# Kernel tuning notes

Measured on AMD Instinct MI355X. Metric: run time of the kernel, lower is better.

## Reference

```python
import jax, jax.numpy as jnp
import numpy as np

THRESHOLD = 0.2  # relation_threshold default
LN_EPS = 1e-5


def setup_inputs() -> dict:
    key = jax.random.key(0)
    ks = jax.random.split(key, 4)
    N1, N2, F, H, R = 256, 256, 512, 512, 4
    feats_img = jax.random.normal(ks[0], (N1, F), dtype=jnp.float32)
    feats_txt = jax.random.normal(ks[1], (N2, F), dtype=jnp.float32)
    # relation_projector params (R stacked copies of the 2-layer MLP)
    W1 = jax.random.normal(ks[2], (R, H, 2 * F), dtype=jnp.float32) / np.sqrt(2 * F)
    b1 = jnp.zeros((R, H), dtype=jnp.float32)
    gamma = jnp.ones((R, H), dtype=jnp.float32)
    beta = jnp.zeros((R, H), dtype=jnp.float32)
    w2 = jax.random.normal(ks[3], (R, H), dtype=jnp.float32) / np.sqrt(H)
    b2 = jnp.zeros((R,), dtype=jnp.float32)
    return {"feats_img": feats_img, "feats_txt": feats_txt, "W1": W1, "b1": b1,
            "gamma": gamma, "beta": beta, "w2": w2, "b2": b2}


def _relation_scores(x, W1, b1, gamma, beta, w2, b2):
    """Vectorized pairwise MLP: for each relation r, score[i,j] = MLP_r(cat(x_i, x_j)).
    Returns [N, N, R]."""
    N, F = x.shape
    R = W1.shape[0]
    Wl, Wr = W1[:, :, :F], W1[:, :, F:]  # Linear on concat = left half @ x_i + right half @ x_j
    scores = []
    for r in range(R):  # small fixed loop over relations keeps peak memory at one [N,N,H] block
        a = x @ Wl[r].T                                  # [N, H]
        b = x @ Wr[r].T                                  # [N, H]
        h = a[:, None, :] + b[None, :, :] + b1[r]        # [N, N, H]
        mu = h.mean(-1, keepdims=True)
        var = h.var(-1, keepdims=True)                   # biased var, matches torch LayerNorm
        hn = (h - mu) * jax.lax.rsqrt(var + LN_EPS) * gamma[r] + beta[r]
        s = jnp.maximum(hn, 0.0) @ w2[r] + b2[r]         # [N, N]
        scores.append(s)
    return jnp.stack(scores, axis=-1)                    # [N, N, R]


def reference(feats_img, feats_txt, W1, b1, gamma, beta, w2, b2):
    # node_features = cat over modalities (node_types is a static host-side list: omitted)
    x = jnp.concatenate([feats_img, feats_txt], axis=0)  # [N, F]
    S = _relation_scores(x, W1, b1, gamma, beta, w2, b2) # [N, N, R]
    best_rel = jnp.argmax(S, axis=-1).astype(jnp.int32)  # edge_types, dense form
    best_score = S.max(axis=-1)                          # edge_weights, dense form
    N = x.shape[0]
    diag = jnp.eye(N, dtype=bool)
    edge_mask = (~diag) & (best_score > THRESHOLD)       # dense encoding of edge_index
    return x, best_score, best_rel, edge_mask
```

## Files before the change

### kernel.cpp

```cpp
#include <hip/hip_runtime.h>
#include <math.h>


typedef __attribute__((ext_vector_type(8))) short s8b;
typedef __attribute__((ext_vector_type(4))) float f32x4;
typedef __attribute__((ext_vector_type(4))) unsigned short us4;

namespace {
constexpr size_t PLANE  = 512 * 512;
constexpr size_t OFF_A   = 0;
constexpr size_t OFF_B   = OFF_A + 4 * PLANE;
constexpr size_t OFF_DOT = OFF_B + 4 * PLANE;
constexpr size_t OFF_S   = OFF_DOT + 8 * PLANE;
constexpr size_t OFF_MA  = OFF_S + 8 * PLANE;
constexpr size_t OFF_QA  = OFF_MA + 2048;
constexpr size_t OFF_MB  = OFF_QA + 2048;
constexpr size_t OFF_QB  = OFF_MB + 2048;
constexpr size_t OFF_G   = OFF_QB + 2048;
constexpr size_t OFF_BW  = OFF_G + 2048;
constexpr size_t OFF_SA  = OFF_BW + 4096;
constexpr size_t OFF_SB  = OFF_SA + 2048;
constexpr size_t OFF_CB  = OFF_SB + 2048;
}

__device__ __forceinline__ unsigned short bf16rne(float v) {
  const unsigned u = __float_as_uint(v);
  return (unsigned short)((u + 0x7fffu + ((u >> 16) & 1u)) >> 16);
}

__device__ __forceinline__ f32x4 mfma16(s8b a, s8b b, f32x4 c) {
  return __builtin_amdgcn_mfma_f32_16x16x32_bf16(a, b, c, 0, 0, 0);
}

__global__ __launch_bounds__(256) void k0_gemm(const float* __restrict__ img,
                                               const float* __restrict__ txt,
                                               const float* __restrict__ W1,
                                               const float* __restrict__ b1,
                                               float* __restrict__ ws) {
  const int b = blockIdx.x;
  const int it = b >> 6;
  const int ct = b & 63;
  const int which = ct >> 5;
  const int r = (ct >> 3) & 3;
  const int ht = ct & 7;
  const int i0 = it << 6, h0 = ht << 6;
  const int t = threadIdx.x;
  const int tx = t & 15, ty = t >> 4;

  __shared__ float Xs[16 * 68];
  __shared__ float Wsm[16 * 68];

  float acc[16], pacc[16];
#pragma unroll
  for (int p = 0; p < 16; ++p) { acc[p] = 0.f; pacc[p] = 0.f; }

  const int srow = t >> 2;
  const int sf4 = (t & 3) << 2;
  const int xi = i0 + srow;
  const float* xrow = (xi < 256) ? (img + (size_t)xi * 512)
                                 : (txt + (size_t)(xi - 256) * 512);
  const float* wrow = W1 + (size_t)(r * 512 + h0 + srow) * 1024 + which * 512;

  for (int k0 = 0; k0 < 512; k0 += 16) {
    const float4 xv = *(const float4*)(xrow + k0 + sf4);
    const float4 wv = *(const float4*)(wrow + k0 + sf4);
    __syncthreads();
    Xs[(sf4 + 0) * 68 + srow] = xv.x;
    Xs[(sf4 + 1) * 68 + srow] = xv.y;
    Xs[(sf4 + 2) * 68 + srow] = xv.z;
    Xs[(sf4 + 3) * 68 + srow] = xv.w;
    Wsm[(sf4 + 0) * 68 + srow] = wv.x;
    Wsm[(sf4 + 1) * 68 + srow] = wv.y;
    Wsm[(sf4 + 2) * 68 + srow] = wv.z;
    Wsm[(sf4 + 3) * 68 + srow] = wv.w;
    __syncthreads();
#pragma unroll
    for (int k = 0; k < 16; ++k) {
      const float4 a4 = *(const float4*)&Xs[k * 68 + 4 * ty];
      const float4 b4 = *(const float4*)&Wsm[k * 68 + 4 * tx];
      const float av[4] = {a4.x, a4.y, a4.z, a4.w};
      const float bv[4] = {b4.x, b4.y, b4.z, b4.w};
#pragma unroll
      for (int c = 0; c < 4; ++c)
#pragma unroll
        for (int d = 0; d < 4; ++d)
          pacc[c * 4 + d] = fmaf(av[c], bv[d], pacc[c * 4 + d]);
    }
#pragma unroll
    for (int p = 0; p < 16; ++p) { acc[p] += pacc[p]; pacc[p] = 0.f; }
  }

  float4 bb = make_float4(0.f, 0.f, 0.f, 0.f);
  if (which) bb = *(const float4*)(b1 + r * 512 + h0 + 4 * tx);
  float* dst = ws + (which ? OFF_B : OFF_A) + (size_t)r * PLANE;
#pragma unroll
  for (int c = 0; c < 4; ++c) {
    float4 v;
    v.x = acc[c * 4 + 0] + bb.x;
    v.y = acc[c * 4 + 1] + bb.y;
    v.z = acc[c * 4 + 2] + bb.z;
    v.w = acc[c * 4 + 3] + bb.w;
    *(float4*)(dst + (size_t)(i0 + 4 * ty + c) * 512 + h0 + 4 * tx) = v;
  }
}

__global__ __launch_bounds__(256) void k_conv2(float* __restrict__ ws) {
  const int idx = blockIdx.x * 256 + threadIdx.x;
  const float4 v = *(const float4*)(ws + (size_t)idx * 4);
  unsigned short* SH = (unsigned short*)(ws + OFF_S);
  unsigned short *dh, *dl;
  if (idx < 262144) {
    const size_t e = (size_t)idx * 4;
    dh = SH + e;                 dl = SH + 4 * PLANE + e;
  } else {
    const size_t e = (size_t)idx * 4 - 4 * PLANE;
    dh = SH + 8 * PLANE + e;     dl = SH + 12 * PLANE + e;
  }
  const float vv[4] = {v.x, v.y, v.z, v.w};
  us4 h4, l4;
#pragma unroll
  for (int c = 0; c < 4; ++c) {
    const unsigned short hh = bf16rne(vv[c]);
    h4[c] = hh;
    l4[c] = bf16rne(vv[c] - __uint_as_float(((unsigned)hh) << 16));
  }
  *(us4*)dh = h4;
  *(us4*)dl = l4;
}

__global__ __launch_bounds__(256) void k1_stats(float* __restrict__ ws,
                                                const float* __restrict__ gamma,
                                                const float* __restrict__ beta,
                                                const float* __restrict__ w2) {
  const int t = threadIdx.x;
  const int gw = (blockIdx.x * 256 + t) >> 6;
  const int lane = t & 63;
  const int which = gw >> 11;
  const int rr = (gw >> 9) & 3;
  const int row = gw & 511;
  const float* src =
      ws + (which ? OFF_B : OFF_A) + (size_t)(rr * 512 + row) * 512 + lane * 8;
  const float* gsrc = gamma + rr * 512 + lane * 8;
  const float* wsrc = w2 + rr * 512 + lane * 8;
  float s = 0.f, q = 0.f, sa = 0.f, cgs = 0.f;
#pragma unroll
  for (int c = 0; c < 2; ++c) {
    const float4 v = *(const float4*)(src + c * 4);
    const float4 g = *(const float4*)(gsrc + c * 4);
    const float4 w = *(const float4*)(wsrc + c * 4);
    s += v.x + v.y + v.z + v.w;
    q += v.x * v.x + v.y * v.y + v.z * v.z + v.w * v.w;
    const float cgx = 0.5f * w.x * g.x;
    const float cgy = 0.5f * w.y * g.y;
    const float cgz = 0.5f * w.z * g.z;
    const float cgw = 0.5f * w.w * g.w;
    sa += cgx * v.x + cgy * v.y + cgz * v.z + cgw * v.w;
    cgs += cgx + cgy + cgz + cgw;
  }
#pragma unroll
  for (int off = 32; off >= 1; off >>= 1) {
    s += __shfl_down(s, off, 64);
    q += __shfl_down(q, off, 64);
    sa += __shfl_down(sa, off, 64);
    cgs += __shfl_down(cgs, off, 64);
  }
  if (lane == 0) {
    const float ma = s * (1.f / 512.f);
    ws[(which ? OFF_MB : OFF_MA) + rr * 512 + row] = ma;
    ws[(which ? OFF_QB : OFF_QA) + rr * 512 + row] = q;
    ws[(which ? OFF_SB : OFF_SA) + rr * 512 + row] = sa - ma * cgs;
  }
  if (blockIdx.x < 8) {
    const int idx = blockIdx.x * 256 + t;
    ws[OFF_G + idx] = gamma[idx];
    float2 bw;
    bw.x = beta[idx];
    bw.y = 0.5f * w2[idx];
    *(float2*)(ws + OFF_BW + (size_t)idx * 2) = bw;
  }
  if (blockIdx.x == 8) {
    const int rb = t >> 6;
    float cb = 0.f;
#pragma unroll
    for (int c = 0; c < 8; ++c)
      cb += 0.5f * w2[rb * 512 + lane * 8 + c] * beta[rb * 512 + lane * 8 + c];
#pragma unroll
    for (int off = 32; off >= 1; off >>= 1) cb += __shfl_down(cb, off, 64);
    if (lane == 0) ws[OFF_CB + rb] = cb;
  }
}

__global__ __launch_bounds__(256) void k2_mfma(float* __restrict__ ws) {
  const int b = blockIdx.x;
  const int jt = b & 7, it = (b >> 3) & 7, r = (b >> 6) & 3, ks = b >> 8;
  const int i0 = it << 6, j0 = jt << 6;
  const int kb = ks << 8;
  const int t = threadIdx.x, w = t >> 6, l = t & 63;
  const int wr = w >> 1, wc = w & 1;
  const int lrow = l & 15, lk = (l >> 4) << 3;

  const unsigned short* SH = (const unsigned short*)(ws + OFF_S);
  const unsigned short* AH = SH;
  const unsigned short* AL = SH + 4 * PLANE;
  const unsigned short* BH = SH + 8 * PLANE;
  const unsigned short* BL = SH + 12 * PLANE;

  const int ia = i0 + wr * 32 + lrow;
  const int jb = j0 + wc * 32 + lrow;
  const size_t ar0 = (size_t)(r * 512 + ia) * 512 + kb + lk;
  const size_t ar1 = ar0 + 16 * 512;
  const size_t br0 = (size_t)(r * 512 + jb) * 512 + kb + lk;
  const size_t br1 = br0 + 16 * 512;

  f32x4 acc00 = {0.f, 0.f, 0.f, 0.f}, acc01 = acc00, acc10 = acc00, acc11 = acc00;

#pragma unroll
  for (int k0 = 0; k0 < 256; k0 += 32) {
    const s8b ah0 = *(const s8b*)(AH + ar0 + k0);
    const s8b ah1 = *(const s8b*)(AH + ar1 + k0);
    const s8b al0 = *(const s8b*)(AL + ar0 + k0);
    const s8b al1 = *(const s8b*)(AL + ar1 + k0);
    const s8b bh0 = *(const s8b*)(BH + br0 + k0);
    const s8b bh1 = *(const s8b*)(BH + br1 + k0);
    const s8b bl0 = *(const s8b*)(BL + br0 + k0);
    const s8b bl1 = *(const s8b*)(BL + br1 + k0);
    acc00 = mfma16(ah0, bh0, acc00);
    acc00 = mfma16(ah0, bl0, acc00);
    acc00 = mfma16(al0, bh0, acc00);
    acc01 = mfma16(ah0, bh1, acc01);
    acc01 = mfma16(ah0, bl1, acc01);
    acc01 = mfma16(al0, bh1, acc01);
    acc10 = mfma16(ah1, bh0, acc10);
    acc10 = mfma16(ah1, bl0, acc10);
    acc10 = mfma16(al1, bh0, acc10);
    acc11 = mfma16(ah1, bh1, acc11);
    acc11 = mfma16(ah1, bl1, acc11);
    acc11 = mfma16(al1, bh1, acc11);
  }

  float* dst = ws + OFF_DOT + (size_t)ks * (4 * PLANE) + (size_t)r * PLANE;
  const int rb = i0 + wr * 32 + ((l >> 4) << 2);
  const int cb = j0 + wc * 32 + lrow;
#pragma unroll
  for (int v = 0; v < 4; ++v) {
    dst[(size_t)(rb + v) * 512 + cb]           = acc00[v];
    dst[(size_t)(rb + v) * 512 + cb + 16]      = acc01[v];
    dst[(size_t)(rb + 16 + v) * 512 + cb]      = acc10[v];
    dst[(size_t)(rb + 16 + v) * 512 + cb + 16] = acc11[v];
  }
}

__global__ __launch_bounds__(256) void k3_score(float* __restrict__ ws) {
  const int b = blockIdx.x;
  const int jt = b & 15, it = (b >> 4) & 7, r = (b >> 7) & 3, ks = b >> 9;
  const int i0 = it << 6, j0 = jt << 5;
  const int t = threadIdx.x;
  const int tx = t & 15, ty = t >> 4;

  __shared__ float As2[64 * 68];
  __shared__ float Bs2[64 * 36];
  __shared__ float bwS[64 * 2];

  const float4 mav = *(const float4*)(ws + OFF_MA + r * 512 + i0 + 4 * ty);
  const float4 qav = *(const float4*)(ws + OFF_QA + r * 512 + i0 + 4 * ty);
  const float2 mbv = *(const float2*)(ws + OFF_MB + r * 512 + j0 + 2 * tx);
  const float2 qbv = *(const float2*)(ws + OFF_QB + r * 512 + j0 + 2 * tx);
  const float4 sav = *(const float4*)(ws + OFF_SA + r * 512 + i0 + 4 * ty);
  const float2 sbv = *(const float2*)(ws + OFF_SB + r * 512 + j0 + 2 * tx);
  const float cbr = ws[OFF_CB + r];
  const float mavA[4] = {mav.x, mav.y, mav.z, mav.w};
  const float qavA[4] = {qav.x, qav.y, qav.z, qav.w};
  const float savA[4] = {sav.x, sav.y, sav.z, sav.w};
  const float mbA[2] = {mbv.x, mbv.y};
  const float qbA[2] = {qbv.x, qbv.y};
  const float sbA[2] = {sbv.x, sbv.y};
  float Sv[8], acc[8];
#pragma unroll
  for (int c = 0; c < 4; ++c) {
    const size_t doff = (size_t)r * PLANE + (size_t)(i0 + 4 * ty + c) * 512 + j0 + 2 * tx;
    const float2 d0 = *(const float2*)(ws + OFF_DOT + doff);
    const float2 d1 = *(const float2*)(ws + OFF_DOT + 4 * PLANE + doff);
    const float dA[2] = {d0.x + d1.x, d0.y + d1.y};
#pragma unroll
    for (int d = 0; d < 2; ++d) {
      const int p = c * 2 + d;
      const float mu = mavA[c] + mbA[d];
      const float msq = (qavA[c] + qbA[d] + 2.f * dA[d]) * (1.f / 512.f);
      const float var = msq - mu * mu;
      Sv[p] = 1.0f / sqrtf(var + 1e-5f);
      acc[p] = (ks == 0) ? fmaf(Sv[p], savA[c] + sbA[d], cbr) : 0.f;
    }
  }

  const int kbase = ks << 8;
  const int srow = ty;
  const int sf4 = tx << 2;
  const int sblk = tx & 7;
  float maR[4], mbR[2];
#pragma unroll
  for (int c2 = 0; c2 < 4; ++c2)
    maR[c2] = ws[OFF_MA + r * 512 + i0 + srow + 16 * c2];
#pragma unroll
  for (int c2 = 0; c2 < 2; ++c2)
    mbR[c2] = ws[OFF_MB + r * 512 + j0 + srow + 16 * c2];

  float4 aC[4], bC[2], gC;
  float2 bwC = make_float2(0.f, 0.f);
  {
    const int kb = kbase;
    gC = *(const float4*)(ws + OFF_G + r * 512 + kb + sf4);
#pragma unroll
    for (int c2 = 0; c2 < 4; ++c2)
      aC[c2] = *(const float4*)(ws + OFF_A + (size_t)(r * 512 + i0 + srow + 16 * c2) * 512 + kb + sf4);
#pragma unroll
    for (int c2 = 0; c2 < 2; ++c2)
      bC[c2] = *(const float4*)(ws + OFF_B + (size_t)(r * 512 + j0 + srow + 16 * c2) * 512 + kb + sf4);
    if (t < 64) bwC = *(const float2*)(ws + OFF_BW + (size_t)(r * 512 + kb + t) * 2);
  }

#pragma unroll
  for (int kc = 0; kc < 4; ++kc) {
    __syncthreads();
    {
      const float ga[4] = {gC.x, gC.y, gC.z, gC.w};
#pragma unroll
      for (int c2 = 0; c2 < 4; ++c2) {
        const int row = srow + 16 * c2;
        const int off = (((row >> 2) ^ sblk) << 2) + (row & 3);
        const float aq[4] = {aC[c2].x, aC[c2].y, aC[c2].z, aC[c2].w};
#pragma unroll
        for (int q = 0; q < 4; ++q)
          As2[(sf4 + q) * 68 + off] = (aq[q] - maR[c2]) * ga[q];
      }
#pragma unroll
      for (int c2 = 0; c2 < 2; ++c2) {
        const int row = srow + 16 * c2;
        const int off = (((row >> 2) ^ sblk) << 2) + (row & 3);
        const float bq[4] = {bC[c2].x, bC[c2].y, bC[c2].z, bC[c2].w};
#pragma unroll
        for (int q = 0; q < 4; ++q)
          Bs2[(sf4 + q) * 36 + off] = (bq[q] - mbR[c2]) * ga[q];
      }
      if (t < 64) *(float2*)(bwS + 2 * t) = bwC;
    }
    if (kc < 3) {
      const int kb = kbase + ((kc + 1) << 6);
      gC = *(const float4*)(ws + OFF_G + r * 512 + kb + sf4);
#pragma unroll
      for (int c2 = 0; c2 < 4; ++c2)
        aC[c2] = *(const float4*)(ws + OFF_A + (size_t)(r * 512 + i0 + srow + 16 * c2) * 512 + kb + sf4);
#pragma unroll
      for (int c2 = 0; c2 < 2; ++c2)
        bC[c2] = *(const float4*)(ws + OFF_B + (size_t)(r * 512 + j0 + srow + 16 * c2) * 512 + kb + sf4);
      if (t < 64) bwC = *(const float2*)(ws + OFF_BW + (size_t)(r * 512 + kb + t) * 2);
    }
    __syncthreads();

    float cacc[8];
#pragma unroll
    for (int p = 0; p < 8; ++p) cacc[p] = 0.f;

#pragma unroll 4
    for (int k = 0; k < 64; ++k) {
      const int K = (k >> 2) & 7;
      const float4 aA = *(const float4*)&As2[k * 68 + ((ty ^ K) << 2)];
      const float2 bB = *(const float2*)&Bs2[k * 36 + (((tx >> 1) ^ K) << 2) + ((tx & 1) << 1)];
      const float2 bw = *(const float2*)&bwS[2 * k];
      const float aq[4] = {aA.x, aA.y, aA.z, aA.w};
      const float bq[2] = {bB.x, bB.y};
#pragma unroll
      for (int c = 0; c < 4; ++c)
#pragma unroll
        for (int d = 0; d < 2; ++d) {
          const int p = c * 2 + d;
          const float u = aq[c] + bq[d];
          const float hn = fmaf(u, Sv[p], bw.x);
          cacc[p] = fmaf(bw.y, fabsf(hn), cacc[p]);
        }
    }
#pragma unroll
    for (int p = 0; p < 8; ++p) acc[p] += cacc[p];
  }

  float* dst = ws + OFF_S + (size_t)ks * (4 * PLANE) + (size_t)r * PLANE;
#pragma unroll
  for (int c = 0; c < 4; ++c) {
    float2 v;
    v.x = acc[c * 2 + 0];
    v.y = acc[c * 2 + 1];
    *(float2*)(dst + (size_t)(i0 + 4 * ty + c) * 512 + j0 + 2 * tx) = v;
  }
}

__global__ __launch_bounds__(256) void k4_combine(const float* __restrict__ ws,
                                                  const float* __restrict__ img,
                                                  const float* __restrict__ txt,
                                                  const float* __restrict__ b2,
                                                  float* __restrict__ out) {
  const int idx = blockIdx.x * 256 + threadIdx.x;
  const int i = idx >> 9, j = idx & 511;
  const float* s0 = ws + OFF_S;
  const float* s1 = ws + OFF_S + 4 * PLANE;
  float best = -3.4e38f;
  int rel = 0;
#pragma unroll
  for (int r = 0; r < 4; ++r) {
    const float s = s0[r * PLANE + idx] + s1[r * PLANE + idx] + b2[r];
    if (s > best) { best = s; rel = r; }
  }
  out[idx] = (i < 256) ? img[idx] : txt[idx - 131072];
  out[PLANE + idx] = best;
  out[2 * PLANE + idx] = (float)rel;
  out[3 * PLANE + idx] = (i != j && (double)best > 0.2) ? 1.0f : 0.0f;
}

extern "C" void kernel_launch(void* const* d_in, const int* in_sizes, int n_in,
                              void* d_out, int out_size, void* d_ws, size_t ws_size,
                              hipStream_t stream) {
  const float* img   = (const float*)d_in[0];
  const float* txt   = (const float*)d_in[1];
  const float* W1    = (const float*)d_in[2];
  const float* b1    = (const float*)d_in[3];
  const float* gamma = (const float*)d_in[4];
  const float* beta  = (const float*)d_in[5];
  const float* w2    = (const float*)d_in[6];
  const float* b2    = (const float*)d_in[7];
  float* ws  = (float*)d_ws;
  float* out = (float*)d_out;
  (void)in_sizes; (void)n_in; (void)out_size; (void)ws_size;

  hipLaunchKernelGGL(k0_gemm,    dim3(512),  dim3(256), 0, stream, img, txt, W1, b1, ws);
  hipLaunchKernelGGL(k_conv2,    dim3(2048), dim3(256), 0, stream, ws);
  hipLaunchKernelGGL(k1_stats,   dim3(1024), dim3(256), 0, stream, ws, gamma, beta, w2);
  hipLaunchKernelGGL(k2_mfma,    dim3(512),  dim3(256), 0, stream, ws);
  hipLaunchKernelGGL(k3_score,   dim3(1024), dim3(256), 0, stream, ws);
  hipLaunchKernelGGL(k4_combine, dim3(1024), dim3(256), 0, stream, ws, img, txt, b2, out);
}
```

Baseline: 192.7 us.

## Replace FP32 projection GEMM with split-bf16 MFMA and fuse hi/lo conversion

The scalar FP32 shared-memory GEMM that computes the left and right projections is replaced by a bf16 MFMA kernel. The inputs are split three ways (hi/mid/lo) and six cross-product MFMAs are accumulated to approximate FP32 accuracy. The kernel writes the hi/lo bf16 split of its outputs directly, so the separate conversion pass over the projections is dropped. In exchange it adds pre-conversion kernels for W1 and x that write extra bf16 planes to the workspace, and runs the projection as two launches, one per half of W1.

```diff
diff --git a/kernel.cpp b/kernel.cpp
--- a/kernel.cpp
+++ b/kernel.cpp
@@ -32,100 +32,160 @@
   return __builtin_amdgcn_mfma_f32_16x16x32_bf16(a, b, c, 0, 0, 0);
 }
 
-__global__ __launch_bounds__(256) void k0_gemm(const float* __restrict__ img,
-                                               const float* __restrict__ txt,
-                                               const float* __restrict__ W1,
-                                               const float* __restrict__ b1,
-                                               float* __restrict__ ws) {
-  const int b = blockIdx.x;
-  const int it = b >> 6;
-  const int ct = b & 63;
-  const int which = ct >> 5;
-  const int r = (ct >> 3) & 3;
-  const int ht = ct & 7;
-  const int i0 = it << 6, h0 = ht << 6;
-  const int t = threadIdx.x;
-  const int tx = t & 15, ty = t >> 4;
-
-  __shared__ float Xs[16 * 68];
-  __shared__ float Wsm[16 * 68];
-
-  float acc[16], pacc[16];
-#pragma unroll
-  for (int p = 0; p < 16; ++p) { acc[p] = 0.f; pacc[p] = 0.f; }
-
-  const int srow = t >> 2;
-  const int sf4 = (t & 3) << 2;
-  const int xi = i0 + srow;
-  const float* xrow = (xi < 256) ? (img + (size_t)xi * 512)
-                                 : (txt + (size_t)(xi - 256) * 512);
-  const float* wrow = W1 + (size_t)(r * 512 + h0 + srow) * 1024 + which * 512;
-
-  for (int k0 = 0; k0 < 512; k0 += 16) {
-    const float4 xv = *(const float4*)(xrow + k0 + sf4);
-    const float4 wv = *(const float4*)(wrow + k0 + sf4);
-    __syncthreads();
-    Xs[(sf4 + 0) * 68 + srow] = xv.x;
-    Xs[(sf4 + 1) * 68 + srow] = xv.y;
-    Xs[(sf4 + 2) * 68 + srow] = xv.z;
-    Xs[(sf4 + 3) * 68 + srow] = xv.w;
-    Wsm[(sf4 + 0) * 68 + srow] = wv.x;
-    Wsm[(sf4 + 1) * 68 + srow] = wv.y;
-    Wsm[(sf4 + 2) * 68 + srow] = wv.z;
-    Wsm[(sf4 + 3) * 68 + srow] = wv.w;
-    __syncthreads();
-#pragma unroll
-    for (int k = 0; k < 16; ++k) {
-      const float4 a4 = *(const float4*)&Xs[k * 68 + 4 * ty];
-      const float4 b4 = *(const float4*)&Wsm[k * 68 + 4 * tx];
-      const float av[4] = {a4.x, a4.y, a4.z, a4.w};
-      const float bv[4] = {b4.x, b4.y, b4.z, b4.w};
-#pragma unroll
-      for (int c = 0; c < 4; ++c)
-#pragma unroll
-        for (int d = 0; d < 4; ++d)
-          pacc[c * 4 + d] = fmaf(av[c], bv[d], pacc[c * 4 + d]);
-    }
-#pragma unroll
-    for (int p = 0; p < 16; ++p) { acc[p] += pacc[p]; pacc[p] = 0.f; }
-  }
-
-  float4 bb = make_float4(0.f, 0.f, 0.f, 0.f);
-  if (which) bb = *(const float4*)(b1 + r * 512 + h0 + 4 * tx);
-  float* dst = ws + (which ? OFF_B : OFF_A) + (size_t)r * PLANE;
-#pragma unroll
-  for (int c = 0; c < 4; ++c) {
-    float4 v;
-    v.x = acc[c * 4 + 0] + bb.x;
-    v.y = acc[c * 4 + 1] + bb.y;
-    v.z = acc[c * 4 + 2] + bb.z;
-    v.w = acc[c * 4 + 3] + bb.w;
-    *(float4*)(dst + (size_t)(i0 + 4 * ty + c) * 512 + h0 + 4 * tx) = v;
-  }
-}
-
-__global__ __launch_bounds__(256) void k_conv2(float* __restrict__ ws) {
+__global__ __launch_bounds__(256) void k_conv1a(const float* __restrict__ img,
+                                                const float* __restrict__ txt,
+                                                const float* __restrict__ W1,
+                                                float* __restrict__ ws) {
   const int idx = blockIdx.x * 256 + threadIdx.x;
-  const float4 v = *(const float4*)(ws + (size_t)idx * 4);
-  unsigned short* SH = (unsigned short*)(ws + OFF_S);
-  unsigned short *dh, *dl;
+  unsigned short* WPH = (unsigned short*)(ws + OFF_DOT);
+  float4 v;
+  size_t off;
+  unsigned short *dh, *dm, *dl;
   if (idx < 262144) {
-    const size_t e = (size_t)idx * 4;
-    dh = SH + e;                 dl = SH + 4 * PLANE + e;
+    const int row = idx >> 7, c4 = (idx & 127) << 2;
+    v = *(const float4*)(W1 + (size_t)row * 1024 + c4);
+    off = (size_t)row * 512 + c4;
+    dh = WPH; dm = WPH + 4 * PLANE; dl = WPH + 8 * PLANE;
   } else {
-    const size_t e = (size_t)idx * 4 - 4 * PLANE;
-    dh = SH + 8 * PLANE + e;     dl = SH + 12 * PLANE + e;
+    const int xi = idx - 262144;
+    v = (xi < 32768) ? ((const float4*)img)[xi] : ((const float4*)txt)[xi - 32768];
+    off = (size_t)xi * 4;
+    dh = WPH + 12 * PLANE; dm = WPH + 13 * PLANE; dl = WPH + 14 * PLANE;
   }
   const float vv[4] = {v.x, v.y, v.z, v.w};
-  us4 h4, l4;
+  us4 h4, m4, l4;
 #pragma unroll
   for (int c = 0; c < 4; ++c) {
     const unsigned short hh = bf16rne(vv[c]);
+    const float r1 = vv[c] - __uint_as_float(((unsigned)hh) << 16);
+    const unsigned short mm = bf16rne(r1);
+    const float r2 = r1 - __uint_as_float(((unsigned)mm) << 16);
     h4[c] = hh;
-    l4[c] = bf16rne(vv[c] - __uint_as_float(((unsigned)hh) << 16));
-  }
-  *(us4*)dh = h4;
-  *(us4*)dl = l4;
+    m4[c] = mm;
+    l4[c] = bf16rne(r2);
+  }
+  *(us4*)(dh + off) = h4;
+  *(us4*)(dm + off) = m4;
+  *(us4*)(dl + off) = l4;
+}
+
+__global__ __launch_bounds__(256) void k_conv1b(const float* __restrict__ W1,
+                                                float* __restrict__ ws) {
+  const int idx = blockIdx.x * 256 + threadIdx.x;
+  unsigned short* WPH = (unsigned short*)(ws + OFF_DOT);
+  const int row = idx >> 7, c4 = (idx & 127) << 2;
+  const float4 v = *(const float4*)(W1 + (size_t)row * 1024 + 512 + c4);
+  const size_t off = (size_t)row * 512 + c4;
+  const float vv[4] = {v.x, v.y, v.z, v.w};
+  us4 h4, m4, l4;
+#pragma unroll
+  for (int c = 0; c < 4; ++c) {
+    const unsigned short hh = bf16rne(vv[c]);
+    const float r1 = vv[c] - __uint_as_float(((unsigned)hh) << 16);
+    const unsigned short mm = bf16rne(r1);
+    const float r2 = r1 - __uint_as_float(((unsigned)mm) << 16);
+    h4[c] = hh;
+    m4[c] = mm;
+    l4[c] = bf16rne(r2);
+  }
+  *(us4*)(WPH + off) = h4;
+  *(us4*)(WPH + 4 * PLANE + off) = m4;
+  *(us4*)(WPH + 8 * PLANE + off) = l4;
+}
+
+__global__ __launch_bounds__(256) void k0_mfma(const float* __restrict__ b1,
+                                               float* __restrict__ ws, int which) {
+  const int b = blockIdx.x;
+  const int it = b >> 5, ct = b & 31;
+  const int r = ct >> 3, ht = ct & 7;
+  const int i0 = it << 6, h0 = ht << 6;
+  const int t = threadIdx.x, w = t >> 6, l = t & 63;
+  const int wr = w >> 1, wc = w & 1;
+  const int lrow = l & 15, lk = (l >> 4) << 3;
+
+  const unsigned short* WPH = (const unsigned short*)(ws + OFF_DOT);
+  const unsigned short* WPM = WPH + 4 * PLANE;
+  const unsigned short* WPL = WPH + 8 * PLANE;
+  const unsigned short* XPH = WPH + 12 * PLANE;
+  const unsigned short* XPM = WPH + 13 * PLANE;
+  const unsigned short* XPL = WPH + 14 * PLANE;
+
+  const int ia = i0 + wr * 32 + lrow;
+  const int hb = h0 + wc * 32 + lrow;
+  const size_t xr0 = (size_t)ia * 512 + lk;
+  const size_t xr1 = xr0 + 16 * 512;
+  const size_t wr0 = (size_t)(r * 512 + hb) * 512 + lk;
+  const size_t wr1 = wr0 + 16 * 512;
+
+  f32x4 acc00 = {0.f, 0.f, 0.f, 0.f}, acc01 = acc00, acc10 = acc00, acc11 = acc00;
+
+#pragma unroll 4
+  for (int k0 = 0; k0 < 512; k0 += 32) {
+    const s8b xh0 = *(const s8b*)(XPH + xr0 + k0);
+    const s8b xh1 = *(const s8b*)(XPH + xr1 + k0);
+    const s8b xm0 = *(const s8b*)(XPM + xr0 + k0);
+    const s8b xm1 = *(const s8b*)(XPM + xr1 + k0);
+    const s8b xl0 = *(const s8b*)(XPL + xr0 + k0);
+    const s8b xl1 = *(const s8b*)(XPL + xr1 + k0);
+    const s8b wh0 = *(const s8b*)(WPH + wr0 + k0);
+    const s8b wh1 = *(const s8b*)(WPH + wr1 + k0);
+    const s8b wm0 = *(const s8b*)(WPM + wr0 + k0);
+    const s8b wm1 = *(const s8b*)(WPM + wr1 + k0);
+    const s8b wl0 = *(const s8b*)(WPL + wr0 + k0);
+    const s8b wl1 = *(const s8b*)(WPL + wr1 + k0);
+    acc00 = mfma16(xh0, wh0, acc00);
+    acc00 = mfma16(xh0, wm0, acc00);
+    acc00 = mfma16(xm0, wh0, acc00);
+    acc00 = mfma16(xh0, wl0, acc00);
+    acc00 = mfma16(xm0, wm0, acc00);
+    acc00 = mfma16(xl0, wh0, acc00);
+    acc01 = mfma16(xh0, wh1, acc01);
+    acc01 = mfma16(xh0, wm1, acc01);
+    acc01 = mfma16(xm0, wh1, acc01);
+    acc01 = mfma16(xh0, wl1, acc01);
+    acc01 = mfma16(xm0, wm1, acc01);
+    acc01 = mfma16(xl0, wh1, acc01);
+    acc10 = mfma16(xh1, wh0, acc10);
+    acc10 = mfma16(xh1, wm0, acc10);
+    acc10 = mfma16(xm1, wh0, acc10);
+    acc10 = mfma16(xh1, wl0, acc10);
+    acc10 = mfma16(xm1, wm0, acc10);
+    acc10 = mfma16(xl1, wh0, acc10);
+    acc11 = mfma16(xh1, wh1, acc11);
+    acc11 = mfma16(xh1, wm1, acc11);
+    acc11 = mfma16(xm1, wh1, acc11);
+    acc11 = mfma16(xh1, wl1, acc11);
+    acc11 = mfma16(xm1, wm1, acc11);
+    acc11 = mfma16(xl1, wh1, acc11);
+  }
+
+  float bb0 = 0.f, bb1 = 0.f;
+  if (which) { bb0 = b1[r * 512 + hb]; bb1 = b1[r * 512 + hb + 16]; }
+  float* dst = ws + (which ? OFF_B : OFF_A) + (size_t)r * PLANE;
+  unsigned short* SHb = (unsigned short*)(ws + OFF_S) + (which ? 8 * PLANE : 0);
+  const int rb = i0 + wr * 32 + ((l >> 4) << 2);
+  const int cb = h0 + wc * 32 + lrow;
+#pragma unroll
+  for (int v = 0; v < 4; ++v) {
+    const float v00 = acc00[v] + bb0;
+    const float v01 = acc01[v] + bb1;
+    const float v10 = acc10[v] + bb0;
+    const float v11 = acc11[v] + bb1;
+    const size_t e00 = (size_t)(rb + v) * 512 + cb;
+    const size_t e01 = e00 + 16;
+    const size_t e10 = (size_t)(rb + 16 + v) * 512 + cb;
+    const size_t e11 = e10 + 16;
+    dst[e00] = v00; dst[e01] = v01; dst[e10] = v10; dst[e11] = v11;
+    const size_t rp = (size_t)r * PLANE;
+    const float vs[4] = {v00, v01, v10, v11};
+    const size_t es[4] = {rp + e00, rp + e01, rp + e10, rp + e11};
+#pragma unroll
+    for (int q = 0; q < 4; ++q) {
+      const unsigned short hh = bf16rne(vs[q]);
+      SHb[es[q]] = hh;
+      SHb[4 * PLANE + es[q]] = bf16rne(vs[q] - __uint_as_float(((unsigned)hh) << 16));
+    }
+  }
 }
 
 __global__ __launch_bounds__(256) void k1_stats(float* __restrict__ ws,
@@ -429,8 +489,10 @@
   float* out = (float*)d_out;
   (void)in_sizes; (void)n_in; (void)out_size; (void)ws_size;
 
-  hipLaunchKernelGGL(k0_gemm,    dim3(512),  dim3(256), 0, stream, img, txt, W1, b1, ws);
-  hipLaunchKernelGGL(k_conv2,    dim3(2048), dim3(256), 0, stream, ws);
+  hipLaunchKernelGGL(k_conv1a,   dim3(1280), dim3(256), 0, stream, img, txt, W1, ws);
+  hipLaunchKernelGGL(k0_mfma,    dim3(256),  dim3(256), 0, stream, b1, ws, 0);
+  hipLaunchKernelGGL(k_conv1b,   dim3(1024), dim3(256), 0, stream, W1, ws);
+  hipLaunchKernelGGL(k0_mfma,    dim3(256),  dim3(256), 0, stream, b1, ws, 1);
   hipLaunchKernelGGL(k1_stats,   dim3(1024), dim3(256), 0, stream, ws, gamma, beta, w2);
   hipLaunchKernelGGL(k2_mfma,    dim3(512),  dim3(256), 0, stream, ws);
   hipLaunchKernelGGL(k3_score,   dim3(1024), dim3(256), 0, stream, ws);
```

Measured after the change: 212.7 us. 1.1x slower.
